# Kernel optimization log

Hardware: AMD Instinct MI355X
Metric: run time of the kernel (lower is better)

Reference implementation:

```python
import jax, jax.numpy as jnp
import numpy as np

T, B, LAG, H = 128, 1024, 6, 256


def setup_inputs() -> dict:
    key = jax.random.key(0)
    ks = jax.random.split(key, 16)
    s = 0.05  # small init scale to keep LSTM gates in a sane range
    d = {}
    d["x"] = jax.random.normal(ks[0], (T, B, LAG), jnp.float32)
    d["Wi1"] = jax.random.normal(ks[1], (H, LAG), jnp.float32) * s
    d["bi1"] = jnp.zeros((H,), jnp.float32)
    d["Wi2"] = jax.random.normal(ks[2], (H, H), jnp.float32) * s
    d["bi2"] = jnp.zeros((H,), jnp.float32)
    d["Wi3"] = jax.random.normal(ks[3], (H, H), jnp.float32) * s
    d["bi3"] = jnp.zeros((H,), jnp.float32)
    d["Wih0"] = jax.random.normal(ks[4], (4 * H, H), jnp.float32) * s
    d["Whh0"] = jax.random.normal(ks[5], (4 * H, H), jnp.float32) * s
    d["bih0"] = jnp.zeros((4 * H,), jnp.float32)
    d["bhh0"] = jnp.zeros((4 * H,), jnp.float32)
    d["Wih1"] = jax.random.normal(ks[6], (4 * H, H), jnp.float32) * s
    d["Whh1"] = jax.random.normal(ks[7], (4 * H, H), jnp.float32) * s
    d["bih1"] = jnp.zeros((4 * H,), jnp.float32)
    d["bhh1"] = jnp.zeros((4 * H,), jnp.float32)
    d["Wo1"] = jax.random.normal(ks[8], (H, H), jnp.float32) * s
    d["bo1"] = jnp.zeros((H,), jnp.float32)
    d["Wo2"] = jax.random.normal(ks[9], (H, H), jnp.float32) * s
    d["bo2"] = jnp.zeros((H,), jnp.float32)
    d["Wo3"] = jax.random.normal(ks[10], (LAG, H), jnp.float32) * s
    d["bo3"] = jnp.zeros((LAG,), jnp.float32)
    return d


def _lstm_cell(xt, h, c, Wih, Whh, bih, bhh):
    # PyTorch gate order: i, f, g, o
    g = xt @ Wih.T + h @ Whh.T + (bih + bhh)
    i, f, gg, o = jnp.split(g, 4, axis=-1)
    c2 = jax.nn.sigmoid(f) * c + jax.nn.sigmoid(i) * jnp.tanh(gg)
    h2 = jax.nn.sigmoid(o) * jnp.tanh(c2)
    return h2, c2


def reference(x, Wi1, bi1, Wi2, bi2, Wi3, bi3,
              Wih0, Whh0, bih0, bhh0, Wih1, Whh1, bih1, bhh1,
              Wo1, bo1, Wo2, bo2, Wo3, bo3):
    relu = jax.nn.relu
    # input MLP applied to every timestep at once: [T,B,6] -> [T,B,H]
    u = relu(x @ Wi1.T + bi1)
    u = relu(u @ Wi2.T + bi2)
    u = relu(u @ Wi3.T + bi3)

    def step(carry, xt):
        h0, c0, h1, c1 = carry
        h0, c0 = _lstm_cell(xt, h0, c0, Wih0, Whh0, bih0, bhh0)
        # dropout(0.05) between layers is identity in eval mode
        h1, c1 = _lstm_cell(h0, h1, c1, Wih1, Whh1, bih1, bhh1)
        return (h0, c0, h1, c1), h1

    z = jnp.zeros((x.shape[1], Whh0.shape[1]), x.dtype)
    _, hs = jax.lax.scan(step, (z, z, z, z), u)  # hs: [T,B,H]

    # output MLP: ReLU, Linear, ReLU, Linear, ReLU, Linear(H->6)
    y = relu(hs)
    y = relu(y @ Wo1.T + bo1)
    y = relu(y @ Wo2.T + bo2)
    y = y @ Wo3.T + bo3
    return y  # [T,B,6]
```

## Files before the change

kernel.cpp:

```cpp
#include <hip/hip_runtime.h>
#include <math.h>


namespace {
constexpr int kT   = 128;
constexpr int kB   = 1024;
constexpr int kLag = 6;
constexpr int kH   = 256;
constexpr int kTc  = 32;
constexpr int kMc  = kTc * kB;
constexpr int kGS  = 132;
constexpr int kLdsForce = 98304;
constexpr int kRankMain = 4096;
constexpr int kCntUints = 16384;
}

typedef _Float16 half8 __attribute__((ext_vector_type(8)));
typedef _Float16 half4 __attribute__((ext_vector_type(4)));
typedef float f32x4 __attribute__((ext_vector_type(4)));
typedef unsigned long long u64;

__device__ __forceinline__ float sigm(float x) {
    return 1.f / (1.f + exp2f(-1.4426950408889634f * x));
}
__device__ __forceinline__ float tanh_(float x) {
    return 2.f / (1.f + exp2f(-2.8853900817779268f * x)) - 1.f;
}

__device__ __forceinline__ half8 pack(u64 a, u64 b) {
    union { u64 u[2]; half8 h; } r;
    r.u[0] = a; r.u[1] = b;
    return r.h;
}

__device__ __forceinline__ void ld_l2(half8& d, const _Float16* p) {
    asm volatile("global_load_dwordx4 %0, %1, off sc0"
                 : "=v"(d) : "v"(p) : "memory");
}
#define WAITCNT_HOLD4(A, B)                                                   \
    asm volatile("s_waitcnt vmcnt(0)"                                         \
        : "+v"(A[0]), "+v"(A[1]), "+v"(B[0]), "+v"(B[1]))

__global__ __launch_bounds__(256)
void zero_fill(unsigned int* __restrict__ p)
{
    p[blockIdx.x * 256 + threadIdx.x] = 0u;
}

__global__ __launch_bounds__(256)
void cvt_f2h(const float* __restrict__ s, _Float16* __restrict__ d)
{
    const int i = blockIdx.x * 256 + threadIdx.x;
    d[i] = (_Float16)s[i];
}

__global__ __launch_bounds__(256)
void build_wcat3(const float* __restrict__ Wih, const float* __restrict__ Whh,
                 _Float16* __restrict__ d)
{
    const int i = blockIdx.x * 256 + threadIdx.x;
    const int row = i >> 9, col = i & 511;
    const int src = (row & 3) * 256 + (row >> 2);
    const float v = (col < 256) ? Wih[src * 256 + col] : Whh[src * 256 + col - 256];
    d[i] = (_Float16)v;
}

__global__ __launch_bounds__(256)
void add_bias(const float* __restrict__ a, const float* __restrict__ b,
              float* __restrict__ d)
{
    const int i = blockIdx.x * 256 + threadIdx.x;
    d[i] = a[i] + b[i];
}

__global__ __launch_bounds__(256)
void in_mlp1(const float* __restrict__ x, const float* __restrict__ Wi1,
             const float* __restrict__ bi1, _Float16* __restrict__ out)
{
    const int idx = blockIdx.x * 256 + threadIdx.x;
    const int col = idx & (kH - 1);
    const int row = idx >> 8;
    const float* xr = x + (size_t)row * kLag;
    const float* w  = Wi1 + col * kLag;
    float s = bi1[col];
#pragma unroll
    for (int k = 0; k < kLag; ++k) s = fmaf(xr[k], w[k], s);
    out[idx] = (_Float16)fmaxf(s, 0.f);
}

__global__ __launch_bounds__(256)
void gemm_h16(const _Float16* __restrict__ A, const _Float16* __restrict__ W,
              const float* __restrict__ bias, _Float16* __restrict__ C)
{
    const int tid = threadIdx.x;
    const int w = tid >> 6, lane = tid & 63, q = lane >> 4, l15 = lane & 15;
    const int n0 = blockIdx.x * 64;
    const int r0 = blockIdx.y * 128 + w * 32;

    half8 bf[4][8];
#pragma unroll
    for (int nt = 0; nt < 4; ++nt)
#pragma unroll
        for (int kk = 0; kk < 8; ++kk)
            bf[nt][kk] = *(const half8*)(W + (size_t)(n0 + nt * 16 + l15) * 256
                                         + kk * 32 + q * 8);
    float bz[4];
#pragma unroll
    for (int nt = 0; nt < 4; ++nt) bz[nt] = bias[n0 + nt * 16 + l15];

#pragma unroll
    for (int rt = 0; rt < 2; ++rt) {
        const _Float16* arow = A + (size_t)(r0 + rt * 16 + l15) * 256 + q * 8;
        half8 af[8];
#pragma unroll
        for (int kk = 0; kk < 8; ++kk) af[kk] = *(const half8*)(arow + kk * 32);
        f32x4 acc[4];
#pragma unroll
        for (int nt = 0; nt < 4; ++nt)
            acc[nt] = (f32x4){bz[nt], bz[nt], bz[nt], bz[nt]};
#pragma unroll
        for (int kk = 0; kk < 8; ++kk)
#pragma unroll
            for (int nt = 0; nt < 4; ++nt)
                acc[nt] = __builtin_amdgcn_mfma_f32_16x16x32_f16(
                    af[kk], bf[nt][kk], acc[nt], 0, 0, 0);
#pragma unroll
        for (int nt = 0; nt < 4; ++nt)
#pragma unroll
            for (int r = 0; r < 4; ++r) {
                const float v = fmaxf(acc[nt][r], 0.f);
                C[(size_t)(r0 + rt * 16 + q * 4 + r) * 256 + n0 + nt * 16 + l15]
                    = (_Float16)v;
            }
    }
}

__device__ __forceinline__ void waitpeers(const unsigned int* __restrict__ fb,
                                          unsigned int target, int tid)
{
    if (tid < 64) {
        const unsigned int* fp = fb + (tid & 7) * 16;
        unsigned int v;
        do {
            v = __hip_atomic_load(fp, __ATOMIC_RELAXED,
                                  __HIP_MEMORY_SCOPE_AGENT);
        } while (__any(v < target));
    }
    __syncthreads();
}

__device__ __forceinline__ void gather_lo(const _Float16* lo, int row, int q,
                                          u64* ua)
{
    const u64* plo = (const u64*)(lo + (size_t)row * 256 + q * 8);
#pragma unroll
    for (int kk = 0; kk < 8; ++kk) {
        ua[2*kk]   = plo[kk*8];
        ua[2*kk+1] = plo[kk*8 + 1];
    }
}

__device__ __forceinline__ void gstore(float* __restrict__ gl, int rt, int wl,
                                       int q, int l15,
                                       const f32x4& a0, const f32x4& a1)
{
#pragma unroll
    for (int r = 0; r < 4; ++r) {
        gl[(rt*16 + q*4 + r) * kGS + wl*32 + l15]      = a0[r];
        gl[(rt*16 + q*4 + r) * kGS + wl*32 + 16 + l15] = a1[r];
    }
}

__device__ __forceinline__ void cells_wave(const float* __restrict__ gl,
    int grow, int gcb, const float* __restrict__ bs, float* __restrict__ cst,
    _Float16* __restrict__ hout, _Float16* __restrict__ uout)
{
    const float* gr = gl + grow * kGS + gcb;
    half4 hv;
#pragma unroll
    for (int c = 0; c < 4; ++c) {
        const f32x4 g4 = *(const f32x4*)(gr + c * 4);
        const float gi = g4[0] + bs[c*4 + 0];
        const float gf = g4[1] + bs[c*4 + 1];
        const float gg = g4[2] + bs[c*4 + 2];
        const float go = g4[3] + bs[c*4 + 3];
        const float c2 = sigm(gf) * cst[c] + sigm(gi) * tanh_(gg);
        cst[c] = c2;
        hv[c] = (_Float16)(sigm(go) * tanh_(c2));
    }
    *(half4*)hout = hv;
    if (uout) {
        const _Float16 z = (_Float16)0.f;
        half4 uv;
#pragma unroll
        for (int c = 0; c < 4; ++c) uv[c] = hv[c] > z ? hv[c] : z;
        *(half4*)uout = uv;
    }
}

__global__ __launch_bounds__(512, 2)
void lstm_all(_Float16* __restrict__ ubuf,
              const _Float16* __restrict__ Wc0, const _Float16* __restrict__ Wc1,
              const float* __restrict__ bc0, const float* __restrict__ bc1,
              _Float16* __restrict__ h0b, _Float16* __restrict__ h1b,
              unsigned int* __restrict__ cnt)
{
    extern __shared__ char lds[];
    char* pH0  = lds;
    char* pH1  = lds + 16384;
    float* gl0 = (float*)(lds + 32768);
    float* gl1 = gl0 + 32 * kGS;

    const int tid = threadIdx.x;
    const int w = tid >> 6, lane = tid & 63, q = lane >> 4, l15 = lane & 15;
    const int wl = w & 3;
    const int lyr = (w < 4) ? 1 : 0;

    __shared__ int sh_bi, sh_js;
    if (tid == 0) {
        unsigned int xcd = __builtin_amdgcn_s_getreg(20 | (31 << 11)) & 7u;
        unsigned int rank = __hip_atomic_fetch_add(cnt + kRankMain + xcd * 16, 1u,
            __ATOMIC_RELAXED, __HIP_MEMORY_SCOPE_AGENT);
        sh_bi = (int)(xcd * 4 + (rank >> 3));
        sh_js = (int)(rank & 7);
    }
    __syncthreads();
    const int bi = sh_bi, js = sh_js;
    unsigned int* fb    = cnt + (size_t)bi * 128;
    unsigned int* fslot = fb + js * 16;

    const _Float16* WcL = lyr ? Wc1 : Wc0;
    half8 Bf0[16], Bf1[16];
    {
        const _Float16* wr0 = WcL + (size_t)(js*128 + wl*32 + l15) * 512 + q * 8;
        const _Float16* wr1 = wr0 + (size_t)16 * 512;
#pragma unroll
        for (int kk = 0; kk < 16; ++kk) {
            Bf0[kk] = *(const half8*)(wr0 + kk * 32);
            Bf1[kk] = *(const half8*)(wr1 + kk * 32);
        }
    }

    int sdst[2];
#pragma unroll
    for (int r = 0; r < 2; ++r) {
        const int L   = tid * 16 + r * 8192;
        const int row = L >> 9;
        const int c   = L & 511;
        sdst[r] = row * 512 + (c ^ ((row & 15) << 4) ^ ((row & 1) << 8));
    }

    const int grow = lane >> 1;
    const int gcb  = wl*32 + (lane & 1) * 16;
    const int hcb  = js*32 + wl*8 + (lane & 1) * 4;
    const float* bcL = lyr ? bc1 : bc0;
    float bs[16];
#pragma unroll
    for (int c = 0; c < 4; ++c)
#pragma unroll
        for (int g = 0; g < 4; ++g)
            bs[c*4 + g] = bcL[g * 256 + hcb + c];
    float cst[4] = {0.f, 0.f, 0.f, 0.f};
    const size_t rbase = (size_t)bi * 32 * 256;
    const size_t coff  = rbase + (size_t)grow * 256 + hcb;

    if (lyr == 0) {
#pragma unroll
        for (int rt = 0; rt < 2; ++rt) {
            u64 ua[16];
            gather_lo(ubuf + rbase, rt*16 + l15, q, ua);
            f32x4 a0 = {0.f,0.f,0.f,0.f}, a1 = {0.f,0.f,0.f,0.f};
#pragma unroll
            for (int kk = 0; kk < 8; ++kk) {
                const half8 af = pack(ua[2*kk], ua[2*kk+1]);
                a0 = __builtin_amdgcn_mfma_f32_16x16x32_f16(af, Bf0[kk], a0, 0,0,0);
                a1 = __builtin_amdgcn_mfma_f32_16x16x32_f16(af, Bf1[kk], a1, 0,0,0);
            }
            gstore(gl0, rt, wl, q, l15, a0, a1);
        }
        cells_wave(gl0, grow, gcb, bs, cst, (_Float16*)(h0b + coff), nullptr);
    }
    asm volatile("s_waitcnt vmcnt(0)" ::: "memory");
    __syncthreads();
    if (tid == 0)
        __hip_atomic_fetch_add(fslot, 1u, __ATOMIC_RELAXED,
                               __HIP_MEMORY_SCOPE_AGENT);

    for (int t = 0; t < kT; ++t) {
        const size_t p  = (size_t)(t & 1) * kB * 256;
        const size_t pn = (size_t)((t & 1) ^ 1) * kB * 256;
        const bool hasB = (t < kT - 1);

        f32x4 aA0 = {0.f,0.f,0.f,0.f}, aA1 = {0.f,0.f,0.f,0.f};
        f32x4 aB0 = {0.f,0.f,0.f,0.f}, aB1 = {0.f,0.f,0.f,0.f};
        if (lyr == 0 && hasB) {
            const _Float16* u = ubuf + (size_t)(t + 1) * kB * 256 + rbase;
            {
                const _Float16* pu = u + (size_t)(l15) * 256 + q * 8;
                half8 uf[8];
#pragma unroll
                for (int kk = 0; kk < 8; ++kk) uf[kk] = *(const half8*)(pu + kk * 32);
#pragma unroll
                for (int kk = 0; kk < 8; ++kk) {
                    aA0 = __builtin_amdgcn_mfma_f32_16x16x32_f16(uf[kk], Bf0[kk], aA0, 0,0,0);
                    aA1 = __builtin_amdgcn_mfma_f32_16x16x32_f16(uf[kk], Bf1[kk], aA1, 0,0,0);
                }
            }
            {
                const _Float16* pu = u + (size_t)(16 + l15) * 256 + q * 8;
                half8 uf[8];
#pragma unroll
                for (int kk = 0; kk < 8; ++kk) uf[kk] = *(const half8*)(pu + kk * 32);
#pragma unroll
                for (int kk = 0; kk < 8; ++kk) {
                    aB0 = __builtin_amdgcn_mfma_f32_16x16x32_f16(uf[kk], Bf0[kk], aB0, 0,0,0);
                    aB1 = __builtin_amdgcn_mfma_f32_16x16x32_f16(uf[kk], Bf1[kk], aB1, 0,0,0);
                }
            }
        }

        waitpeers(fb, (unsigned)(t + 1), tid);

        {
            half8 s0[2], s1h[2];
            const char* b0 = (const char*)(h0b + p  + rbase);
            const char* b1 = (const char*)(h1b + pn + rbase);
#pragma unroll
            for (int r = 0; r < 2; ++r) {
                ld_l2(s0[r],  (const _Float16*)(b0 + tid * 16 + r * 8192));
                ld_l2(s1h[r], (const _Float16*)(b1 + tid * 16 + r * 8192));
            }
            WAITCNT_HOLD4(s0, s1h);
#pragma unroll
            for (int r = 0; r < 2; ++r) {
                *(half8*)(pH0 + sdst[r]) = s0[r];
                *(half8*)(pH1 + sdst[r]) = s1h[r];
            }
        }
        __syncthreads();

        if (lyr == 1) {
#pragma unroll
            for (int rt = 0; rt < 2; ++rt) {
                const int row = rt*16 + l15;
                const int xr  = ((row & 15) << 4) ^ ((row & 1) << 8);
                const int rb  = row * 512;
                f32x4 a0 = {0.f,0.f,0.f,0.f}, a1 = {0.f,0.f,0.f,0.f};
#pragma unroll
                for (int kk = 0; kk < 8; ++kk) {
                    const int off = rb + ((q * 16 + kk * 64) ^ xr);
                    const half8 alo = *(const half8*)(pH0 + off);
                    const half8 ahi = *(const half8*)(pH1 + off);
                    a0 = __builtin_amdgcn_mfma_f32_16x16x32_f16(alo, Bf0[kk],     a0, 0,0,0);
                    a1 = __builtin_amdgcn_mfma_f32_16x16x32_f16(alo, Bf1[kk],     a1, 0,0,0);
                    a0 = __builtin_amdgcn_mfma_f32_16x16x32_f16(ahi, Bf0[8 + kk], a0, 0,0,0);
                    a1 = __builtin_amdgcn_mfma_f32_16x16x32_f16(ahi, Bf1[8 + kk], a1, 0,0,0);
                }
                gstore(gl1, rt, wl, q, l15, a0, a1);
            }
            cells_wave(gl1, grow, gcb, bs, cst,
                       (_Float16*)(h1b + p + coff),
                       (_Float16*)(ubuf + (size_t)t * kB * 256 + coff));
        } else if (hasB) {
            {
                const int row = l15;
                const int xr  = ((row & 15) << 4) ^ ((row & 1) << 8);
                const int rb  = row * 512;
#pragma unroll
                for (int kk = 0; kk < 8; ++kk) {
                    const int off = rb + ((q * 16 + kk * 64) ^ xr);
                    const half8 ah = *(const half8*)(pH0 + off);
                    aA0 = __builtin_amdgcn_mfma_f32_16x16x32_f16(ah, Bf0[8 + kk], aA0, 0,0,0);
                    aA1 = __builtin_amdgcn_mfma_f32_16x16x32_f16(ah, Bf1[8 + kk], aA1, 0,0,0);
                }
                gstore(gl0, 0, wl, q, l15, aA0, aA1);
            }
            {
                const int row = 16 + l15;
                const int xr  = ((row & 15) << 4) ^ ((row & 1) << 8);
                const int rb  = row * 512;
#pragma unroll
                for (int kk = 0; kk < 8; ++kk) {
                    const int off = rb + ((q * 16 + kk * 64) ^ xr);
                    const half8 ah = *(const half8*)(pH0 + off);
                    aB0 = __builtin_amdgcn_mfma_f32_16x16x32_f16(ah, Bf0[8 + kk], aB0, 0,0,0);
                    aB1 = __builtin_amdgcn_mfma_f32_16x16x32_f16(ah, Bf1[8 + kk], aB1, 0,0,0);
                }
                gstore(gl0, 1, wl, q, l15, aB0, aB1);
            }
            cells_wave(gl0, grow, gcb, bs, cst,
                       (_Float16*)(h0b + pn + coff), nullptr);
        }

        asm volatile("s_waitcnt vmcnt(0)" ::: "memory");
        __syncthreads();
        if (hasB && tid == 0)
            __hip_atomic_fetch_add(fslot, 1u, __ATOMIC_RELAXED,
                                   __HIP_MEMORY_SCOPE_AGENT);
    }
}

__global__ __launch_bounds__(256)
void out_mlp3(const _Float16* __restrict__ y2, const float* __restrict__ Wo3,
              const float* __restrict__ bo3, float* __restrict__ out)
{
    const int lane = threadIdx.x & 63;
    const int row  = blockIdx.x * 4 + (threadIdx.x >> 6);
    const _Float16* yr = y2 + (size_t)row * kH + lane * 4;
    const float a0 = (float)yr[0], a1 = (float)yr[1], a2 = (float)yr[2], a3 = (float)yr[3];
    float s[kLag];
#pragma unroll
    for (int o = 0; o < kLag; ++o) {
        const float4 wv = *(const float4*)(Wo3 + o * kH + lane * 4);
        s[o] = a0 * wv.x + a1 * wv.y + a2 * wv.z + a3 * wv.w;
    }
#pragma unroll
    for (int off = 32; off > 0; off >>= 1) {
#pragma unroll
        for (int o = 0; o < kLag; ++o) s[o] += __shfl_down(s[o], off);
    }
    if (lane == 0) {
#pragma unroll
        for (int o = 0; o < kLag; ++o)
            out[(size_t)row * kLag + o] = s[o] + bo3[o];
    }
}

extern "C" void kernel_launch(void* const* d_in, const int* in_sizes, int n_in,
                              void* d_out, int out_size, void* d_ws, size_t ws_size,
                              hipStream_t stream)
{
    const float* x    = (const float*)d_in[0];
    const float* Wi1  = (const float*)d_in[1];
    const float* bi1  = (const float*)d_in[2];
    const float* Wi2  = (const float*)d_in[3];
    const float* bi2  = (const float*)d_in[4];
    const float* Wi3  = (const float*)d_in[5];
    const float* bi3  = (const float*)d_in[6];
    const float* Wih0 = (const float*)d_in[7];
    const float* Whh0 = (const float*)d_in[8];
    const float* bih0 = (const float*)d_in[9];
    const float* bhh0 = (const float*)d_in[10];
    const float* Wih1 = (const float*)d_in[11];
    const float* Whh1 = (const float*)d_in[12];
    const float* bih1 = (const float*)d_in[13];
    const float* bhh1 = (const float*)d_in[14];
    const float* Wo1  = (const float*)d_in[15];
    const float* bo1  = (const float*)d_in[16];
    const float* Wo2  = (const float*)d_in[17];
    const float* bo2  = (const float*)d_in[18];
    const float* Wo3  = (const float*)d_in[19];
    const float* bo3  = (const float*)d_in[20];
    float* outp = (float*)d_out;

    char* p = (char*)d_ws;
    _Float16* ubuf = (_Float16*)p;  p += (size_t)kT * kB * kH * 2;
    _Float16* s1   = (_Float16*)p;  p += (size_t)kMc * kH * 2;
    _Float16* s2   = (_Float16*)p;  p += (size_t)kMc * kH * 2;
    _Float16* Wc0  = (_Float16*)p;  p += (size_t)1024 * 512 * 2;
    _Float16* Wc1  = (_Float16*)p;  p += (size_t)1024 * 512 * 2;
    _Float16* W2h  = (_Float16*)p;  p += (size_t)kH * kH * 2;
    _Float16* W3h  = (_Float16*)p;  p += (size_t)kH * kH * 2;
    _Float16* Wo1h = (_Float16*)p;  p += (size_t)kH * kH * 2;
    _Float16* Wo2h = (_Float16*)p;  p += (size_t)kH * kH * 2;
    float* bc0 = (float*)p;  p += 1024 * 4;
    float* bc1 = (float*)p;  p += 1024 * 4;
    _Float16* h0b = (_Float16*)p;  p += (size_t)2 * kB * kH * 2;
    _Float16* h1b = (_Float16*)p;  p += (size_t)2 * kB * kH * 2;
    unsigned int* cnt = (unsigned int*)p;  p += kCntUints * 4;

    zero_fill<<<2112, 256, 0, stream>>>((unsigned int*)h0b);
    cvt_f2h<<<kH * kH / 256, 256, 0, stream>>>(Wi2, W2h);
    cvt_f2h<<<kH * kH / 256, 256, 0, stream>>>(Wi3, W3h);
    cvt_f2h<<<kH * kH / 256, 256, 0, stream>>>(Wo1, Wo1h);
    cvt_f2h<<<kH * kH / 256, 256, 0, stream>>>(Wo2, Wo2h);
    build_wcat3<<<1024 * 512 / 256, 256, 0, stream>>>(Wih0, Whh0, Wc0);
    build_wcat3<<<1024 * 512 / 256, 256, 0, stream>>>(Wih1, Whh1, Wc1);
    add_bias<<<4, 256, 0, stream>>>(bih0, bhh0, bc0);
    add_bias<<<4, 256, 0, stream>>>(bih1, bhh1, bc1);

    for (int c = 0; c < kT / kTc; ++c) {
        in_mlp1<<<kMc * kH / 256, 256, 0, stream>>>(
            x + (size_t)c * kMc * kLag, Wi1, bi1, s1);
        gemm_h16<<<dim3(4, kMc / 128), 256, 0, stream>>>(s1, W2h, bi2, s2);
        gemm_h16<<<dim3(4, kMc / 128), 256, 0, stream>>>(
            s2, W3h, bi3, ubuf + (size_t)c * kMc * kH);
    }

    static bool attr_set = false;
    if (!attr_set) {
        hipFuncSetAttribute((const void*)lstm_all,
                            hipFuncAttributeMaxDynamicSharedMemorySize, kLdsForce);
        attr_set = true;
    }
    void* args[] = {&ubuf, &Wc0, &Wc1, &bc0, &bc1, &h0b, &h1b, &cnt};
    hipLaunchCooperativeKernel((const void*)lstm_all, dim3(256), dim3(512),
                               args, kLdsForce, stream);

    for (int c = 0; c < kT / kTc; ++c) {
        gemm_h16<<<dim3(4, kMc / 128), 256, 0, stream>>>(
            ubuf + (size_t)c * kMc * kH, Wo1h, bo1, s1);
        gemm_h16<<<dim3(4, kMc / 128), 256, 0, stream>>>(s1, Wo2h, bo2, s2);
        out_mlp3<<<kMc / 4, 256, 0, stream>>>(
            s2, Wo3, bo3, outp + (size_t)c * kMc * kLag);
    }
}
```

Baseline: 2.091 ms.

## Replace block-wide barrier sync with per-wave flags and direct L2 operand loads

The LSTM persistent kernel no longer stages h0/h1 through LDS with a block-wide __syncthreads per step. Each wave now polls 64 per-wave flags (layer 0 and layer 1 separately) and loads its MFMA operands straight from L2. The layer-0 h buffer becomes triple-buffered so layer 0 can run ahead of layer 1 by one step. This is meant to cut barrier and LDS staging latency from the serial recurrence, at the cost of more atomic polling traffic, redundant global loads per wave, and a larger counter region.

```diff
diff --git a/kernel.cpp b/kernel.cpp
--- a/kernel.cpp
+++ b/kernel.cpp
@@ -11,8 +11,8 @@
 constexpr int kMc  = kTc * kB;
 constexpr int kGS  = 132;
 constexpr int kLdsForce = 98304;
-constexpr int kRankMain = 4096;
-constexpr int kCntUints = 16384;
+constexpr int kRankMain = 32768;
+constexpr int kCntUints = 36864;
 }
 
 typedef _Float16 half8 __attribute__((ext_vector_type(8)));
@@ -27,19 +27,16 @@
     return 2.f / (1.f + exp2f(-2.8853900817779268f * x)) - 1.f;
 }
 
-__device__ __forceinline__ half8 pack(u64 a, u64 b) {
-    union { u64 u[2]; half8 h; } r;
-    r.u[0] = a; r.u[1] = b;
-    return r.h;
-}
-
 __device__ __forceinline__ void ld_l2(half8& d, const _Float16* p) {
     asm volatile("global_load_dwordx4 %0, %1, off sc0"
                  : "=v"(d) : "v"(p) : "memory");
 }
-#define WAITCNT_HOLD4(A, B)                                                   \
+#define WAITCNT_HOLD16(A)                                                     \
     asm volatile("s_waitcnt vmcnt(0)"                                         \
-        : "+v"(A[0]), "+v"(A[1]), "+v"(B[0]), "+v"(B[1]))
+        : "+v"(A[0]), "+v"(A[1]), "+v"(A[2]), "+v"(A[3]),                     \
+          "+v"(A[4]), "+v"(A[5]), "+v"(A[6]), "+v"(A[7]),                     \
+          "+v"(A[8]), "+v"(A[9]), "+v"(A[10]), "+v"(A[11]),                   \
+          "+v"(A[12]), "+v"(A[13]), "+v"(A[14]), "+v"(A[15]))
 
 __global__ __launch_bounds__(256)
 void zero_fill(unsigned int* __restrict__ p)
@@ -135,28 +132,17 @@
     }
 }
 
-__device__ __forceinline__ void waitpeers(const unsigned int* __restrict__ fb,
-                                          unsigned int target, int tid)
-{
-    if (tid < 64) {
-        const unsigned int* fp = fb + (tid & 7) * 16;
-        unsigned int v;
-        do {
-            v = __hip_atomic_load(fp, __ATOMIC_RELAXED,
-                                  __HIP_MEMORY_SCOPE_AGENT);
-        } while (__any(v < target));
-    }
-    __syncthreads();
-}
-
-__device__ __forceinline__ void gather_lo(const _Float16* lo, int row, int q,
-                                          u64* ua)
-{
-    const u64* plo = (const u64*)(lo + (size_t)row * 256 + q * 8);
-#pragma unroll
-    for (int kk = 0; kk < 8; ++kk) {
-        ua[2*kk]   = plo[kk*8];
-        ua[2*kk+1] = plo[kk*8 + 1];
+__device__ __forceinline__ void pollw(const unsigned int* __restrict__ fb,
+                                      unsigned int tlo, unsigned int thi,
+                                      int lane)
+{
+    const unsigned int* fp = fb + lane * 16;
+    const unsigned int tgt = (lane < 32) ? tlo : thi;
+    while (true) {
+        const unsigned int v =
+            __hip_atomic_load(fp, __ATOMIC_RELAXED, __HIP_MEMORY_SCOPE_AGENT);
+        if (!__any(v < tgt)) break;
+        __builtin_amdgcn_s_sleep(1);
     }
 }
 
@@ -168,6 +154,34 @@
     for (int r = 0; r < 4; ++r) {
         gl[(rt*16 + q*4 + r) * kGS + wl*32 + l15]      = a0[r];
         gl[(rt*16 + q*4 + r) * kGS + wl*32 + 16 + l15] = a1[r];
+    }
+}
+
+__device__ __forceinline__ void ugemm(const _Float16* __restrict__ u,
+    const half8 (&B0)[16], const half8 (&B1)[16], int q, int l15,
+    f32x4& aA0, f32x4& aA1, f32x4& aB0, f32x4& aB1)
+{
+    {
+        const _Float16* pu = u + (size_t)l15 * 256 + q * 8;
+        half8 uf[8];
+#pragma unroll
+        for (int kk = 0; kk < 8; ++kk) uf[kk] = *(const half8*)(pu + kk * 32);
+#pragma unroll
+        for (int kk = 0; kk < 8; ++kk) {
+            aA0 = __builtin_amdgcn_mfma_f32_16x16x32_f16(uf[kk], B0[kk], aA0, 0,0,0);
+            aA1 = __builtin_amdgcn_mfma_f32_16x16x32_f16(uf[kk], B1[kk], aA1, 0,0,0);
+        }
+    }
+    {
+        const _Float16* pu = u + (size_t)(16 + l15) * 256 + q * 8;
+        half8 uf[8];
+#pragma unroll
+        for (int kk = 0; kk < 8; ++kk) uf[kk] = *(const half8*)(pu + kk * 32);
+#pragma unroll
+        for (int kk = 0; kk < 8; ++kk) {
+            aB0 = __builtin_amdgcn_mfma_f32_16x16x32_f16(uf[kk], B0[kk], aB0, 0,0,0);
+            aB1 = __builtin_amdgcn_mfma_f32_16x16x32_f16(uf[kk], B1[kk], aB1, 0,0,0);
+        }
     }
 }
 
@@ -206,9 +220,7 @@
               unsigned int* __restrict__ cnt)
 {
     extern __shared__ char lds[];
-    char* pH0  = lds;
-    char* pH1  = lds + 16384;
-    float* gl0 = (float*)(lds + 32768);
+    float* gl0 = (float*)lds;
     float* gl1 = gl0 + 32 * kGS;
 
     const int tid = threadIdx.x;
@@ -226,8 +238,8 @@
     }
     __syncthreads();
     const int bi = sh_bi, js = sh_js;
-    unsigned int* fb    = cnt + (size_t)bi * 128;
-    unsigned int* fslot = fb + js * 16;
+    unsigned int* fb    = cnt + (size_t)bi * 1024;
+    unsigned int* fslot = fb + (lyr ? (32 + js*4 + wl) : (js*4 + wl)) * 16;
 
     const _Float16* WcL = lyr ? Wc1 : Wc0;
     half8 Bf0[16], Bf1[16];
@@ -241,15 +253,6 @@
         }
     }
 
-    int sdst[2];
-#pragma unroll
-    for (int r = 0; r < 2; ++r) {
-        const int L   = tid * 16 + r * 8192;
-        const int row = L >> 9;
-        const int c   = L & 511;
-        sdst[r] = row * 512 + (c ^ ((row & 15) << 4) ^ ((row & 1) << 8));
-    }
-
     const int grow = lane >> 1;
     const int gcb  = wl*32 + (lane & 1) * 16;
     const int hcb  = js*32 + wl*8 + (lane & 1) * 4;
@@ -265,138 +268,94 @@
     const size_t coff  = rbase + (size_t)grow * 256 + hcb;
 
     if (lyr == 0) {
-#pragma unroll
-        for (int rt = 0; rt < 2; ++rt) {
-            u64 ua[16];
-            gather_lo(ubuf + rbase, rt*16 + l15, q, ua);
-            f32x4 a0 = {0.f,0.f,0.f,0.f}, a1 = {0.f,0.f,0.f,0.f};
-#pragma unroll
-            for (int kk = 0; kk < 8; ++kk) {
-                const half8 af = pack(ua[2*kk], ua[2*kk+1]);
-                a0 = __builtin_amdgcn_mfma_f32_16x16x32_f16(af, Bf0[kk], a0, 0,0,0);
-                a1 = __builtin_amdgcn_mfma_f32_16x16x32_f16(af, Bf1[kk], a1, 0,0,0);
-            }
-            gstore(gl0, rt, wl, q, l15, a0, a1);
-        }
+        f32x4 aA0 = {0.f,0.f,0.f,0.f}, aA1 = {0.f,0.f,0.f,0.f};
+        f32x4 aB0 = {0.f,0.f,0.f,0.f}, aB1 = {0.f,0.f,0.f,0.f};
+        ugemm(ubuf + rbase, Bf0, Bf1, q, l15, aA0, aA1, aB0, aB1);
+        gstore(gl0, 0, wl, q, l15, aA0, aA1);
+        gstore(gl0, 1, wl, q, l15, aB0, aB1);
         cells_wave(gl0, grow, gcb, bs, cst, (_Float16*)(h0b + coff), nullptr);
-    }
-    asm volatile("s_waitcnt vmcnt(0)" ::: "memory");
-    __syncthreads();
-    if (tid == 0)
-        __hip_atomic_fetch_add(fslot, 1u, __ATOMIC_RELAXED,
-                               __HIP_MEMORY_SCOPE_AGENT);
-
+        asm volatile("s_waitcnt vmcnt(0)" ::: "memory");
+        if (lane == 0)
+            __hip_atomic_fetch_add(fslot, 1u, __ATOMIC_RELAXED,
+                                   __HIP_MEMORY_SCOPE_AGENT);
+    } else {
+        if (lane == 0)
+            __hip_atomic_fetch_add(fslot, 1u, __ATOMIC_RELAXED,
+                                   __HIP_MEMORY_SCOPE_AGENT);
+    }
+
+    int bufr = 0;
     for (int t = 0; t < kT; ++t) {
+        const size_t b0r = (size_t)bufr * kB * 256;
+        const size_t b0w = (size_t)(bufr == 2 ? 0 : bufr + 1) * kB * 256;
         const size_t p  = (size_t)(t & 1) * kB * 256;
         const size_t pn = (size_t)((t & 1) ^ 1) * kB * 256;
         const bool hasB = (t < kT - 1);
 
-        f32x4 aA0 = {0.f,0.f,0.f,0.f}, aA1 = {0.f,0.f,0.f,0.f};
-        f32x4 aB0 = {0.f,0.f,0.f,0.f}, aB1 = {0.f,0.f,0.f,0.f};
-        if (lyr == 0 && hasB) {
-            const _Float16* u = ubuf + (size_t)(t + 1) * kB * 256 + rbase;
-            {
-                const _Float16* pu = u + (size_t)(l15) * 256 + q * 8;
-                half8 uf[8];
-#pragma unroll
-                for (int kk = 0; kk < 8; ++kk) uf[kk] = *(const half8*)(pu + kk * 32);
+        if (lyr == 1) {
+            pollw(fb, (unsigned)(t + 1), (unsigned)(t + 1), lane);
+            __builtin_amdgcn_sched_barrier(0);
+            const char* h0p = (const char*)(h0b + b0r + rbase);
+            const char* h1p = (const char*)(h1b + pn  + rbase);
+#pragma unroll
+            for (int rt = 0; rt < 2; ++rt) {
+                const int rb = (rt*16 + l15) * 512 + q * 16;
+                half8 A[16];
 #pragma unroll
                 for (int kk = 0; kk < 8; ++kk) {
-                    aA0 = __builtin_amdgcn_mfma_f32_16x16x32_f16(uf[kk], Bf0[kk], aA0, 0,0,0);
-                    aA1 = __builtin_amdgcn_mfma_f32_16x16x32_f16(uf[kk], Bf1[kk], aA1, 0,0,0);
+                    ld_l2(A[kk],     (const _Float16*)(h0p + rb + kk * 64));
+                    ld_l2(A[8 + kk], (const _Float16*)(h1p + rb + kk * 64));
                 }
-            }
-            {
-                const _Float16* pu = u + (size_t)(16 + l15) * 256 + q * 8;
-                half8 uf[8];
-#pragma unroll
-                for (int kk = 0; kk < 8; ++kk) uf[kk] = *(const half8*)(pu + kk * 32);
+                WAITCNT_HOLD16(A);
+                f32x4 a0 = {0.f,0.f,0.f,0.f}, a1 = {0.f,0.f,0.f,0.f};
 #pragma unroll
                 for (int kk = 0; kk < 8; ++kk) {
-                    aB0 = __builtin_amdgcn_mfma_f32_16x16x32_f16(uf[kk], Bf0[kk], aB0, 0,0,0);
-                    aB1 = __builtin_amdgcn_mfma_f32_16x16x32_f16(uf[kk], Bf1[kk], aB1, 0,0,0);
-                }
-            }
-        }
-
-        waitpeers(fb, (unsigned)(t + 1), tid);
-
-        {
-            half8 s0[2], s1h[2];
-            const char* b0 = (const char*)(h0b + p  + rbase);
-            const char* b1 = (const char*)(h1b + pn + rbase);
-#pragma unroll
-            for (int r = 0; r < 2; ++r) {
-                ld_l2(s0[r],  (const _Float16*)(b0 + tid * 16 + r * 8192));
-                ld_l2(s1h[r], (const _Float16*)(b1 + tid * 16 + r * 8192));
-            }
-            WAITCNT_HOLD4(s0, s1h);
-#pragma unroll
-            for (int r = 0; r < 2; ++r) {
-                *(half8*)(pH0 + sdst[r]) = s0[r];
-                *(half8*)(pH1 + sdst[r]) = s1h[r];
-            }
-        }
-        __syncthreads();
-
-        if (lyr == 1) {
-#pragma unroll
-            for (int rt = 0; rt < 2; ++rt) {
-                const int row = rt*16 + l15;
-                const int xr  = ((row & 15) << 4) ^ ((row & 1) << 8);
-                const int rb  = row * 512;
-                f32x4 a0 = {0.f,0.f,0.f,0.f}, a1 = {0.f,0.f,0.f,0.f};
-#pragma unroll
-                for (int kk = 0; kk < 8; ++kk) {
-                    const int off = rb + ((q * 16 + kk * 64) ^ xr);
-                    const half8 alo = *(const half8*)(pH0 + off);
-                    const half8 ahi = *(const half8*)(pH1 + off);
-                    a0 = __builtin_amdgcn_mfma_f32_16x16x32_f16(alo, Bf0[kk],     a0, 0,0,0);
-                    a1 = __builtin_amdgcn_mfma_f32_16x16x32_f16(alo, Bf1[kk],     a1, 0,0,0);
-                    a0 = __builtin_amdgcn_mfma_f32_16x16x32_f16(ahi, Bf0[8 + kk], a0, 0,0,0);
-                    a1 = __builtin_amdgcn_mfma_f32_16x16x32_f16(ahi, Bf1[8 + kk], a1, 0,0,0);
+                    a0 = __builtin_amdgcn_mfma_f32_16x16x32_f16(A[kk], Bf0[kk],         a0, 0,0,0);
+                    a1 = __builtin_amdgcn_mfma_f32_16x16x32_f16(A[kk], Bf1[kk],         a1, 0,0,0);
+                    a0 = __builtin_amdgcn_mfma_f32_16x16x32_f16(A[8 + kk], Bf0[8 + kk], a0, 0,0,0);
+                    a1 = __builtin_amdgcn_mfma_f32_16x16x32_f16(A[8 + kk], Bf1[8 + kk], a1, 0,0,0);
                 }
                 gstore(gl1, rt, wl, q, l15, a0, a1);
             }
             cells_wave(gl1, grow, gcb, bs, cst,
                        (_Float16*)(h1b + p + coff),
                        (_Float16*)(ubuf + (size_t)t * kB * 256 + coff));
+            asm volatile("s_waitcnt vmcnt(0)" ::: "memory");
+            if (lane == 0)
+                __hip_atomic_fetch_add(fslot, 1u, __ATOMIC_RELAXED,
+                                       __HIP_MEMORY_SCOPE_AGENT);
         } else if (hasB) {
-            {
-                const int row = l15;
-                const int xr  = ((row & 15) << 4) ^ ((row & 1) << 8);
-                const int rb  = row * 512;
-#pragma unroll
-                for (int kk = 0; kk < 8; ++kk) {
-                    const int off = rb + ((q * 16 + kk * 64) ^ xr);
-                    const half8 ah = *(const half8*)(pH0 + off);
-                    aA0 = __builtin_amdgcn_mfma_f32_16x16x32_f16(ah, Bf0[8 + kk], aA0, 0,0,0);
-                    aA1 = __builtin_amdgcn_mfma_f32_16x16x32_f16(ah, Bf1[8 + kk], aA1, 0,0,0);
-                }
-                gstore(gl0, 0, wl, q, l15, aA0, aA1);
+            f32x4 aA0 = {0.f,0.f,0.f,0.f}, aA1 = {0.f,0.f,0.f,0.f};
+            f32x4 aB0 = {0.f,0.f,0.f,0.f}, aB1 = {0.f,0.f,0.f,0.f};
+            ugemm(ubuf + (size_t)(t + 1) * kB * 256 + rbase,
+                  Bf0, Bf1, q, l15, aA0, aA1, aB0, aB1);
+            pollw(fb, (unsigned)(t + 1), (unsigned)t, lane);
+            __builtin_amdgcn_sched_barrier(0);
+            const char* h0p = (const char*)(h0b + b0r + rbase);
+            half8 Hh[16];
+#pragma unroll
+            for (int kk = 0; kk < 8; ++kk) {
+                ld_l2(Hh[kk],     (const _Float16*)(h0p + l15 * 512        + q * 16 + kk * 64));
+                ld_l2(Hh[8 + kk], (const _Float16*)(h0p + (16 + l15) * 512 + q * 16 + kk * 64));
             }
-            {
-                const int row = 16 + l15;
-                const int xr  = ((row & 15) << 4) ^ ((row & 1) << 8);
-                const int rb  = row * 512;
-#pragma unroll
-                for (int kk = 0; kk < 8; ++kk) {
-                    const int off = rb + ((q * 16 + kk * 64) ^ xr);
-                    const half8 ah = *(const half8*)(pH0 + off);
-                    aB0 = __builtin_amdgcn_mfma_f32_16x16x32_f16(ah, Bf0[8 + kk], aB0, 0,0,0);
-                    aB1 = __builtin_amdgcn_mfma_f32_16x16x32_f16(ah, Bf1[8 + kk], aB1, 0,0,0);
-                }
-                gstore(gl0, 1, wl, q, l15, aB0, aB1);
+            WAITCNT_HOLD16(Hh);
+#pragma unroll
+            for (int kk = 0; kk < 8; ++kk) {
+                aA0 = __builtin_amdgcn_mfma_f32_16x16x32_f16(Hh[kk], Bf0[8 + kk],     aA0, 0,0,0);
+                aA1 = __builtin_amdgcn_mfma_f32_16x16x32_f16(Hh[kk], Bf1[8 + kk],     aA1, 0,0,0);
+                aB0 = __builtin_amdgcn_mfma_f32_16x16x32_f16(Hh[8 + kk], Bf0[8 + kk], aB0, 0,0,0);
+                aB1 = __builtin_amdgcn_mfma_f32_16x16x32_f16(Hh[8 + kk], Bf1[8 + kk], aB1, 0,0,0);
             }
+            gstore(gl0, 0, wl, q, l15, aA0, aA1);
+            gstore(gl0, 1, wl, q, l15, aB0, aB1);
             cells_wave(gl0, grow, gcb, bs, cst,
-                       (_Float16*)(h0b + pn + coff), nullptr);
+                       (_Float16*)(h0b + b0w + coff), nullptr);
+            asm volatile("s_waitcnt vmcnt(0)" ::: "memory");
+            if (lane == 0)
+                __hip_atomic_fetch_add(fslot, 1u, __ATOMIC_RELAXED,
+                                       __HIP_MEMORY_SCOPE_AGENT);
         }
-
-        asm volatile("s_waitcnt vmcnt(0)" ::: "memory");
-        __syncthreads();
-        if (hasB && tid == 0)
-            __hip_atomic_fetch_add(fslot, 1u, __ATOMIC_RELAXED,
-                                   __HIP_MEMORY_SCOPE_AGENT);
+        bufr = (bufr == 2) ? 0 : bufr + 1;
     }
 }
 
@@ -465,11 +424,11 @@
     _Float16* Wo2h = (_Float16*)p;  p += (size_t)kH * kH * 2;
     float* bc0 = (float*)p;  p += 1024 * 4;
     float* bc1 = (float*)p;  p += 1024 * 4;
-    _Float16* h0b = (_Float16*)p;  p += (size_t)2 * kB * kH * 2;
+    _Float16* h0b = (_Float16*)p;  p += (size_t)3 * kB * kH * 2;
     _Float16* h1b = (_Float16*)p;  p += (size_t)2 * kB * kH * 2;
     unsigned int* cnt = (unsigned int*)p;  p += kCntUints * 4;
 
-    zero_fill<<<2112, 256, 0, stream>>>((unsigned int*)h0b);
+    zero_fill<<<2704, 256, 0, stream>>>((unsigned int*)h0b);
     cvt_f2h<<<kH * kH / 256, 256, 0, stream>>>(Wi2, W2h);
     cvt_f2h<<<kH * kH / 256, 256, 0, stream>>>(Wi3, W3h);
     cvt_f2h<<<kH * kH / 256, 256, 0, stream>>>(Wo1, Wo1h);
```

Result: no change. 2.052 ms (-1.9%).
